# Kernel optimization log

Measured on AMD Instinct MI355X. Metric: run time of the kernel, lower is better.

## Reference

```python
import jax, jax.numpy as jnp
import numpy as np
import math

D_MODEL = 1024
HEADS = 16
D_K = D_MODEL // HEADS
D_FF = 2048
EPS = 1e-6


def layer_norm(x, alpha, bias):
    # torch.std uses unbiased estimator (ddof=1)
    m = x.mean(axis=-1, keepdims=True)
    var = ((x - m) ** 2).sum(axis=-1, keepdims=True) / (x.shape[-1] - 1)
    return alpha * (x - m) / (jnp.sqrt(var) + EPS) + bias


def setup_inputs() -> dict:
    key = jax.random.key(0)
    ks = jax.random.split(key, 12)
    s = 1.0 / math.sqrt(D_MODEL)
    return {
        "x": jax.random.normal(ks[0], (2, 2048, D_MODEL), dtype=jnp.float32),
        "mask": jnp.ones((2, 1, 1, 2048), dtype=jnp.float32),
        "Wq": jax.random.uniform(ks[1], (D_MODEL, D_MODEL), minval=-s, maxval=s),
        "Wk": jax.random.uniform(ks[2], (D_MODEL, D_MODEL), minval=-s, maxval=s),
        "Wv": jax.random.uniform(ks[3], (D_MODEL, D_MODEL), minval=-s, maxval=s),
        "Wo": jax.random.uniform(ks[4], (D_MODEL, D_MODEL), minval=-s, maxval=s),
        "bo": jnp.zeros((D_MODEL,), dtype=jnp.float32),
        "W1": jax.random.uniform(ks[5], (D_MODEL, D_FF), minval=-s, maxval=s),
        "b1": jnp.zeros((D_FF,), dtype=jnp.float32),
        "W2": jax.random.uniform(ks[6], (D_FF, D_MODEL), minval=-1.0 / math.sqrt(D_FF), maxval=1.0 / math.sqrt(D_FF)),
        "b2": jnp.zeros((D_MODEL,), dtype=jnp.float32),
        "ln1_a": jnp.ones((D_MODEL,), dtype=jnp.float32),
        "ln1_b": jnp.zeros((D_MODEL,), dtype=jnp.float32),
        "ln2_a": jnp.ones((D_MODEL,), dtype=jnp.float32),
        "ln2_b": jnp.zeros((D_MODEL,), dtype=jnp.float32),
    }


def reference(x, mask, Wq, Wk, Wv, Wo, bo, W1, b1, W2, b2, ln1_a, ln1_b, ln2_a, ln2_b):
    B, S, _ = x.shape
    # --- attention sublayer (pre-LN) ---
    x2 = layer_norm(x, ln1_a, ln1_b)
    q = (x2 @ Wq).reshape(B, S, HEADS, D_K).transpose(0, 2, 1, 3)  # [B,H,S,dk]
    k = (x2 @ Wk).reshape(B, S, HEADS, D_K).transpose(0, 2, 1, 3)
    v = (x2 @ Wv).reshape(B, S, HEADS, D_K).transpose(0, 2, 1, 3)
    attn = jnp.einsum("bhqd,bhkd->bhqk", q, k) / math.sqrt(D_K)
    attn = attn * mask                                  # multiplicative mask
    attn = jnp.where(attn == 0.0, -jnp.inf, attn)       # masked_fill(==0, -inf)
    scores = jax.nn.softmax(attn, axis=-1)
    av = jnp.einsum("bhqk,bhkd->bhqd", scores, v)
    concat = av.transpose(0, 2, 1, 3).reshape(B, S, D_MODEL)
    x = x + (concat @ Wo + bo)
    # --- FFN sublayer (pre-LN) ---
    x2 = layer_norm(x, ln2_a, ln2_b)
    h = jax.nn.relu(x2 @ W1 + b1)
    x = x + (h @ W2 + b2)
    return x
```

## Files before the change

kernel.cpp:

```cpp
#include <hip/hip_runtime.h>
#include <hip/hip_bf16.h>

typedef unsigned short u16;
typedef __attribute__((ext_vector_type(4))) float f32x4;
typedef __attribute__((ext_vector_type(8))) short bf16x8;

#define SEQ 2048
#define DM 1024
#define DKK 64
#define NH 16
#define DFF 2048
#define TOK 4096

#define AS1 __attribute__((address_space(1)))
#define AS3 __attribute__((address_space(3)))

#define MFMA16(a, b, c) __builtin_amdgcn_mfma_f32_16x16x32_bf16((a), (b), (c), 0, 0, 0)

__device__ __forceinline__ u16 f2b(float f) {
  unsigned u = __float_as_uint(f);
  u = u + 0x7fffu + ((u >> 16) & 1u);
  return (u16)(u >> 16);
}

__device__ __forceinline__ unsigned cvtpk(float lo, float hi) {
  unsigned r;
  asm("v_cvt_pk_bf16_f32 %0, %1, %2" : "=v"(r) : "v"(lo), "v"(hi));
  return r;
}

__device__ __forceinline__ void gload_lds16(const u16* g, u16* l) {
  __builtin_amdgcn_global_load_lds((AS1 unsigned*)(size_t)g, (AS3 unsigned*)l, 16, 0, 0);
}

__global__ __launch_bounds__(256)
void transpose_all(const float* __restrict__ Wq, const float* __restrict__ Wk,
                   const float* __restrict__ Wv, const float* __restrict__ Wo,
                   const float* __restrict__ W1, const float* __restrict__ W2,
                   u16* __restrict__ Wqkt, u16* __restrict__ Wvt, u16* __restrict__ Wot,
                   u16* __restrict__ W1t, u16* __restrict__ W2t) {
  const int bid = blockIdx.x;
  const float* src;
  u16* dst;
  int K, N, lb;
  if (bid < 1024)      { src = Wq; dst = Wqkt;                 K = 1024; N = 1024; lb = bid; }
  else if (bid < 2048) { src = Wk; dst = Wqkt + (1 << 20);     K = 1024; N = 1024; lb = bid - 1024; }
  else if (bid < 3072) { src = Wv; dst = Wvt;                  K = 1024; N = 1024; lb = bid - 2048; }
  else if (bid < 4096) { src = Wo; dst = Wot;                  K = 1024; N = 1024; lb = bid - 3072; }
  else if (bid < 6144) { src = W1; dst = W1t;                  K = 1024; N = 2048; lb = bid - 4096; }
  else                 { src = W2; dst = W2t;                  K = 2048; N = 1024; lb = bid - 6144; }
  const int nx = N / 32;
  const int n0 = (lb % nx) * 32, k0 = (lb / nx) * 32;
  __shared__ float t[32][33];
  const int tx = threadIdx.x, ty = threadIdx.y;
#pragma unroll
  for (int i = 0; i < 4; i++) {
    int k = ty + i * 8;
    t[k][tx] = src[(size_t)(k0 + k) * N + n0 + tx];
  }
  __syncthreads();
#pragma unroll
  for (int i = 0; i < 4; i++) {
    int n = ty + i * 8;
    dst[(size_t)(n0 + n) * K + k0 + tx] = f2b(t[tx][n]);
  }
}

__global__ __launch_bounds__(256)
void ln_kernel(const float* __restrict__ x, const float* __restrict__ alpha,
               const float* __restrict__ beta, u16* __restrict__ out) {
  const int row = blockIdx.x;
  const float4 v = ((const float4*)(x + (size_t)row * DM))[threadIdx.x];
  float s = v.x + v.y + v.z + v.w;
  float q = v.x * v.x + v.y * v.y + v.z * v.z + v.w * v.w;
#pragma unroll
  for (int off = 1; off < 64; off <<= 1) {
    s += __shfl_xor(s, off);
    q += __shfl_xor(q, off);
  }
  __shared__ float ss[4], qq[4];
  const int wid = threadIdx.x >> 6;
  if ((threadIdx.x & 63) == 0) { ss[wid] = s; qq[wid] = q; }
  __syncthreads();
  s = ss[0] + ss[1] + ss[2] + ss[3];
  q = qq[0] + qq[1] + qq[2] + qq[3];
  const float mean = s * (1.f / DM);
  float var = (q - (float)DM * mean * mean) * (1.f / (DM - 1));
  var = fmaxf(var, 0.f);
  const float inv = 1.f / (sqrtf(var) + 1e-6f);
  const float4 a4 = ((const float4*)alpha)[threadIdx.x];
  const float4 b4 = ((const float4*)beta)[threadIdx.x];
  ushort4 o;
  o.x = f2b((v.x - mean) * inv * a4.x + b4.x);
  o.y = f2b((v.y - mean) * inv * a4.y + b4.y);
  o.z = f2b((v.z - mean) * inv * a4.z + b4.z);
  o.w = f2b((v.w - mean) * inv * a4.w + b4.w);
  ((ushort4*)(out + (size_t)row * DM))[threadIdx.x] = o;
}

template <int MODE, int BM, int BN>
__global__ __launch_bounds__(256, 2)
void gemm_bt(const u16* __restrict__ A, const u16* __restrict__ Bt,
             int M, int N, int K,
             const float* __restrict__ bias, const float* __restrict__ res,
             void* __restrict__ outp, float oscale) {
  constexpr int AccM = BM / 32;
  constexpr int AccN = BN / 32;
  constexpr int L = (BM == 128 ? 2 : 1) + (BN == 128 ? 2 : 1);
  __shared__ alignas(16) u16 As[3][BM * 32];
  __shared__ alignas(16) u16 Bs[3][BN * 32];
  const int bm = blockIdx.x * BM, bn = blockIdx.y * BN;
  const int tid = threadIdx.x;
  const int lane = tid & 63, w = tid >> 6;
  const int wm = (w >> 1) * (BM / 2), wn = (w & 1) * (BN / 2);
  const int r = lane & 15, g = lane >> 4;
  const int srow = tid >> 2, skk = (tid & 3) * 8;

  f32x4 acc[AccM][AccN];
#pragma unroll
  for (int i = 0; i < AccM; i++)
#pragma unroll
    for (int j = 0; j < AccN; j++) acc[i][j] = (f32x4){0.f, 0.f, 0.f, 0.f};

  const u16* aP = A + (size_t)(bm + srow) * K + skk;
  const u16* bP = Bt + (size_t)(bn + srow) * K + skk;

  auto stage = [&](int kt, int buf) {
    gload_lds16(aP + kt, &As[buf][0] + w * 512);
    if (BM == 128) gload_lds16(aP + (size_t)64 * K + kt, &As[buf][0] + w * 512 + 2048);
    gload_lds16(bP + kt, &Bs[buf][0] + w * 512);
    if (BN == 128) gload_lds16(bP + (size_t)64 * K + kt, &Bs[buf][0] + w * 512 + 2048);
  };
  auto waitL = [&]() {
    if constexpr (L == 4) asm volatile("s_waitcnt vmcnt(4) lgkmcnt(0)" ::: "memory");
    else if constexpr (L == 3) asm volatile("s_waitcnt vmcnt(3) lgkmcnt(0)" ::: "memory");
    else asm volatile("s_waitcnt vmcnt(2) lgkmcnt(0)" ::: "memory");
  };
  auto compute = [&](int buf) {
    bf16x8 af[AccM], bfr[AccN];
#pragma unroll
    for (int i = 0; i < AccM; i++) af[i] = *(const bf16x8*)(&As[buf][(wm + i * 16 + r) * 32 + g * 8]);
#pragma unroll
    for (int j = 0; j < AccN; j++) bfr[j] = *(const bf16x8*)(&Bs[buf][(wn + j * 16 + r) * 32 + g * 8]);
#pragma unroll
    for (int i = 0; i < AccM; i++)
#pragma unroll
      for (int j = 0; j < AccN; j++) acc[i][j] = MFMA16(af[i], bfr[j], acc[i][j]);
  };

  const int NKT = K / 32;
  stage(0, 0);
  stage(32, 1);
  waitL();
  __builtin_amdgcn_s_barrier();
  __builtin_amdgcn_sched_barrier(0);
  for (int it = 0; it < NKT - 2; ++it) {
    stage((it + 2) * 32, (it + 2) % 3);
    compute(it % 3);
    waitL();
    __builtin_amdgcn_s_barrier();
    __builtin_amdgcn_sched_barrier(0);
  }
  compute((NKT - 2) % 3);
  asm volatile("s_waitcnt vmcnt(0) lgkmcnt(0)" ::: "memory");
  __builtin_amdgcn_s_barrier();
  __builtin_amdgcn_sched_barrier(0);
  compute((NKT - 1) % 3);

#pragma unroll
  for (int i = 0; i < AccM; i++)
#pragma unroll
    for (int j = 0; j < AccN; j++)
#pragma unroll
      for (int t = 0; t < 4; t++) {
        const int mg = bm + wm + i * 16 + g * 4 + t;
        const int ng = bn + wn + j * 16 + r;
        const float v = acc[i][j][t];
        if (MODE == 0) {
          const int which = ng >> 10, col = ng & 1023;
          const int bb = mg >> 11, ssx = mg & 2047, hh = col >> 6, dd = col & 63;
          const float sc = which ? 1.f : oscale;
          ((u16*)outp)[(size_t)which * (TOK * (size_t)DM) +
                       ((size_t)(bb * NH + hh) * SEQ + ssx) * DKK + dd] = f2b(v * sc);
        } else if (MODE == 1) {
          const int hh = mg >> 6, dd = mg & 63, bb = ng >> 11, ssx = ng & 2047;
          ((u16*)outp)[((size_t)(bb * NH + hh) * DKK + dd) * SEQ + ssx] = f2b(v);
        } else if (MODE == 2) {
          ((float*)outp)[(size_t)mg * N + ng] = res[(size_t)mg * N + ng] + v + bias[ng];
        } else {
          const float hv = v + bias[ng];
          ((u16*)outp)[(size_t)mg * N + ng] = f2b(hv > 0.f ? hv : 0.f);
        }
      }
}

__global__ __launch_bounds__(256, 4)
void attn_kernel(const u16* __restrict__ Q, const u16* __restrict__ Kb,
                 const u16* __restrict__ Vt, const float* __restrict__ mask,
                 u16* __restrict__ outc) {
  const int bid = blockIdx.x;
  const int bh = (bid & 7) * 4 + ((bid >> 3) & 3);
  const int qt = bid >> 5;
  const int b = bh >> 4, h = bh & 15;
  const int tid = threadIdx.x, lane = tid & 63, w = tid >> 6;
  const int r = lane & 15, g = lane >> 4;
  const int qbase = qt * 64 + w * 16;
  const u16* Qp = Q + ((size_t)bh * SEQ + qbase) * DKK;
  const u16* Kp = Kb + (size_t)bh * SEQ * DKK;
  const u16* Vp = Vt + (size_t)bh * DKK * SEQ;
  const float* mk = mask + b * SEQ;

  const bf16x8 bq0 = *(const bf16x8*)(Qp + r * DKK + g * 8);
  const bf16x8 bq1 = *(const bf16x8*)(Qp + r * DKK + 32 + g * 8);

  __shared__ __align__(16) u16 Ks[2][64 * 64];
  __shared__ __align__(16) u16 Vs[2][64 * 64];

  const int srow8 = lane >> 3;
  const int sgr = (lane & 7) ^ srow8;
  const u16* kSrc1 = Kp + (size_t)(w * 16 + srow8) * DKK + sgr * 8;
  const u16* kSrc2 = kSrc1 + 8 * DKK;
  const u16* vSrc1 = Vp + (size_t)(w * 16 + srow8) * SEQ + sgr * 8;
  const u16* vSrc2 = vSrc1 + 8 * SEQ;

  f32x4 o[4];
#pragma unroll
  for (int i = 0; i < 4; i++) o[i] = (f32x4){0.f, 0.f, 0.f, 0.f};
  float lr = 0.f;
  const int keyr = r & 7;

  gload_lds16(kSrc1, &Ks[0][0] + w * 1024);
  gload_lds16(kSrc2, &Ks[0][0] + w * 1024 + 512);
  gload_lds16(vSrc1, &Vs[0][0] + w * 1024);
  gload_lds16(vSrc2, &Vs[0][0] + w * 1024 + 512);
  asm volatile("s_waitcnt vmcnt(0)" ::: "memory");
  __builtin_amdgcn_s_barrier();
  __builtin_amdgcn_sched_barrier(0);

  const int NT = SEQ / 64;
  for (int it = 0; it < NT; ++it) {
    const int buf = it & 1;
    if (it + 1 < NT) {
      const int nsk = (it + 1) * 64;
      u16* kd = &Ks[buf ^ 1][0] + w * 1024;
      gload_lds16(kSrc1 + (size_t)nsk * DKK, kd);
      gload_lds16(kSrc2 + (size_t)nsk * DKK, kd + 512);
      u16* vd = &Vs[buf ^ 1][0] + w * 1024;
      gload_lds16(vSrc1 + nsk, vd);
      gload_lds16(vSrc2 + nsk, vd + 512);
    }

    f32x4 s[4];
    __builtin_amdgcn_s_setprio(1);
#pragma unroll
    for (int ks = 0; ks < 4; ks++) {
      const bf16x8 ka0 = *(const bf16x8*)&Ks[buf][(ks * 16 + r) * 64 + ((g ^ keyr) << 3)];
      const bf16x8 ka1 = *(const bf16x8*)&Ks[buf][(ks * 16 + r) * 64 + (((g + 4) ^ keyr) << 3)];
      f32x4 z = (f32x4){0.f, 0.f, 0.f, 0.f};
      z = MFMA16(ka0, bq0, z);
      z = MFMA16(ka1, bq1, z);
      s[ks] = z;
    }
    __builtin_amdgcn_s_setprio(0);

    const int sk = it * 64;
    float p[16];
    float rs = 0.f;
#pragma unroll
    for (int ks = 0; ks < 4; ks++) {
      const float4 mm = *(const float4*)(mk + sk + ks * 16 + 4 * g);
      float pr0 = s[ks][0] * mm.x, pr1 = s[ks][1] * mm.y;
      float pr2 = s[ks][2] * mm.z, pr3 = s[ks][3] * mm.w;
      float e0 = __builtin_amdgcn_exp2f(pr0), e1 = __builtin_amdgcn_exp2f(pr1);
      float e2 = __builtin_amdgcn_exp2f(pr2), e3 = __builtin_amdgcn_exp2f(pr3);
      e0 = (pr0 == 0.f) ? 0.f : e0;
      e1 = (pr1 == 0.f) ? 0.f : e1;
      e2 = (pr2 == 0.f) ? 0.f : e2;
      e3 = (pr3 == 0.f) ? 0.f : e3;
      p[ks * 4 + 0] = e0; p[ks * 4 + 1] = e1; p[ks * 4 + 2] = e2; p[ks * 4 + 3] = e3;
      rs += e0 + e1 + e2 + e3;
    }
    rs += __shfl_xor(rs, 16);
    rs += __shfl_xor(rs, 32);
    lr += rs;

    unsigned wk[4][2];
#pragma unroll
    for (int ks = 0; ks < 4; ks++) {
      wk[ks][0] = cvtpk(p[ks * 4 + 0], p[ks * 4 + 1]);
      wk[ks][1] = cvtpk(p[ks * 4 + 2], p[ks * 4 + 3]);
    }
    bf16x8 pa[2];
#pragma unroll
    for (int hh2 = 0; hh2 < 2; hh2++) {
      union { unsigned u[4]; bf16x8 v; } pu;
#pragma unroll
      for (int c = 0; c < 4; c++) {
        const int srcl = r + ((g & 1) * 2 + (c >> 1)) * 16;
        const unsigned lo = __shfl(wk[2 * hh2][c & 1], srcl);
        const unsigned hi = __shfl(wk[2 * hh2 + 1][c & 1], srcl);
        pu.u[c] = (g < 2) ? lo : hi;
      }
      pa[hh2] = pu.v;
    }

    __builtin_amdgcn_s_setprio(1);
#pragma unroll
    for (int dc = 0; dc < 4; dc++) {
      const int vr = dc * 16 + r;
      const bf16x8 bv0 = *(const bf16x8*)&Vs[buf][vr * 64 + ((g ^ keyr) << 3)];
      const bf16x8 bv1 = *(const bf16x8*)&Vs[buf][vr * 64 + (((g + 4) ^ keyr) << 3)];
      o[dc] = MFMA16(pa[0], bv0, o[dc]);
      o[dc] = MFMA16(pa[1], bv1, o[dc]);
    }
    __builtin_amdgcn_s_setprio(0);

    asm volatile("s_waitcnt vmcnt(0) lgkmcnt(0)" ::: "memory");
    __builtin_amdgcn_s_barrier();
    __builtin_amdgcn_sched_barrier(0);
  }

  float lq[4];
#pragma unroll
  for (int t = 0; t < 4; t++) lq[t] = __shfl(lr, 4 * g + t);
#pragma unroll
  for (int dc = 0; dc < 4; dc++)
#pragma unroll
    for (int t = 0; t < 4; t++) {
      const int srow_g = qbase + g * 4 + t;
      outc[((size_t)(b * SEQ + srow_g)) * DM + h * DKK + dc * 16 + r] = f2b(o[dc][t] / lq[t]);
    }
}

extern "C" void kernel_launch(void* const* d_in, const int* in_sizes, int n_in,
                              void* d_out, int out_size, void* d_ws, size_t ws_size,
                              hipStream_t stream) {
  const float* x    = (const float*)d_in[0];
  const float* mask = (const float*)d_in[1];
  const float* Wq   = (const float*)d_in[2];
  const float* Wk   = (const float*)d_in[3];
  const float* Wv   = (const float*)d_in[4];
  const float* Wo   = (const float*)d_in[5];
  const float* bo   = (const float*)d_in[6];
  const float* W1   = (const float*)d_in[7];
  const float* b1   = (const float*)d_in[8];
  const float* W2   = (const float*)d_in[9];
  const float* b2   = (const float*)d_in[10];
  const float* l1a  = (const float*)d_in[11];
  const float* l1b  = (const float*)d_in[12];
  const float* l2a  = (const float*)d_in[13];
  const float* l2b  = (const float*)d_in[14];

  char* wsb = (char*)d_ws;
  u16* Wqkt = (u16*)(wsb + (0ull << 20));
  u16* Wvt  = (u16*)(wsb + (4ull << 20));
  u16* Wot  = (u16*)(wsb + (6ull << 20));
  u16* W1t  = (u16*)(wsb + (8ull << 20));
  u16* W2t  = (u16*)(wsb + (12ull << 20));
  u16* x2   = (u16*)(wsb + (16ull << 20));
  u16* qkb  = (u16*)(wsb + (24ull << 20));
  u16* vtb  = (u16*)(wsb + (40ull << 20));
  float* x1 = (float*)(wsb + (48ull << 20));
  u16* concat = x2;
  u16* x2b = qkb;
  u16* hb  = (u16*)(wsb + (32ull << 20));

  const float qscale = 0.125f * 1.4426950408889634f;

  transpose_all<<<dim3(8192), dim3(32, 8), 0, stream>>>(Wq, Wk, Wv, Wo, W1, W2,
                                                        Wqkt, Wvt, Wot, W1t, W2t);

  ln_kernel<<<TOK, 256, 0, stream>>>(x, l1a, l1b, x2);

  gemm_bt<0, 128, 128><<<dim3(TOK / 128, 2048 / 128), 256, 0, stream>>>(
      x2, Wqkt, TOK, 2048, DM, nullptr, nullptr, qkb, qscale);
  gemm_bt<1, 64, 128><<<dim3(DM / 64, TOK / 128), 256, 0, stream>>>(
      Wvt, x2, DM, TOK, DM, nullptr, nullptr, vtb, 1.0f);

  attn_kernel<<<dim3(1024), 256, 0, stream>>>(qkb, qkb + (size_t)TOK * DM, vtb, mask, concat);

  gemm_bt<2, 128, 64><<<dim3(TOK / 128, DM / 64), 256, 0, stream>>>(
      concat, Wot, TOK, DM, DM, bo, x, x1, 1.0f);

  ln_kernel<<<TOK, 256, 0, stream>>>(x1, l2a, l2b, x2b);

  gemm_bt<3, 128, 128><<<dim3(TOK / 128, DFF / 128), 256, 0, stream>>>(
      x2b, W1t, TOK, DFF, DM, b1, nullptr, hb, 1.0f);
  gemm_bt<2, 128, 64><<<dim3(TOK / 128, DM / 64), 256, 0, stream>>>(
      hb, W2t, TOK, DM, DFF, b2, x1, (float*)d_out, 1.0f);
}
```

Baseline: 228.5 us.

## Restructure attention as split-K per wave and retile GEMMs with XCD-aware swizzle

```diff
diff --git a/kernel.cpp b/kernel.cpp
--- a/kernel.cpp
+++ b/kernel.cpp
@@ -99,17 +99,20 @@
 }
 
 template <int MODE, int BM, int BN>
-__global__ __launch_bounds__(256, 2)
+__global__ __launch_bounds__(256, 4)
 void gemm_bt(const u16* __restrict__ A, const u16* __restrict__ Bt,
              int M, int N, int K,
              const float* __restrict__ bias, const float* __restrict__ res,
-             void* __restrict__ outp, float oscale) {
+             void* __restrict__ outp, float oscale, int nm) {
   constexpr int AccM = BM / 32;
   constexpr int AccN = BN / 32;
   constexpr int L = (BM == 128 ? 2 : 1) + (BN == 128 ? 2 : 1);
   __shared__ alignas(16) u16 As[3][BM * 32];
   __shared__ alignas(16) u16 Bs[3][BN * 32];
-  const int bm = blockIdx.x * BM, bn = blockIdx.y * BN;
+  const int nwg = gridDim.x;
+  const int cpx = nwg >> 3;
+  const int wg = (blockIdx.x & 7) * cpx + (blockIdx.x >> 3);
+  const int bm = (wg % nm) * BM, bn = (wg / nm) * BN;
   const int tid = threadIdx.x;
   const int lane = tid & 63, w = tid >> 6;
   const int wm = (w >> 1) * (BM / 2), wn = (w & 1) * (BN / 2);
@@ -194,7 +197,7 @@
       }
 }
 
-__global__ __launch_bounds__(256, 4)
+__global__ __launch_bounds__(256, 2)
 void attn_kernel(const u16* __restrict__ Q, const u16* __restrict__ Kb,
                  const u16* __restrict__ Vt, const float* __restrict__ mask,
                  u16* __restrict__ outc) {
@@ -204,132 +207,177 @@
   const int b = bh >> 4, h = bh & 15;
   const int tid = threadIdx.x, lane = tid & 63, w = tid >> 6;
   const int r = lane & 15, g = lane >> 4;
-  const int qbase = qt * 64 + w * 16;
+  const int qbase = qt * 64;
   const u16* Qp = Q + ((size_t)bh * SEQ + qbase) * DKK;
   const u16* Kp = Kb + (size_t)bh * SEQ * DKK;
   const u16* Vp = Vt + (size_t)bh * DKK * SEQ;
-  const float* mk = mask + b * SEQ;
-
-  const bf16x8 bq0 = *(const bf16x8*)(Qp + r * DKK + g * 8);
-  const bf16x8 bq1 = *(const bf16x8*)(Qp + r * DKK + 32 + g * 8);
-
-  __shared__ __align__(16) u16 Ks[2][64 * 64];
-  __shared__ __align__(16) u16 Vs[2][64 * 64];
+  const int wk0 = w * 512;
+  const float* mk = mask + b * SEQ + wk0;
+
+  bf16x8 bq0[4], bq1[4];
+#pragma unroll
+  for (int qf = 0; qf < 4; qf++) {
+    bq0[qf] = *(const bf16x8*)(Qp + (size_t)(qf * 16 + r) * DKK + g * 8);
+    bq1[qf] = *(const bf16x8*)(Qp + (size_t)(qf * 16 + r) * DKK + 32 + g * 8);
+  }
+
+  __shared__ __align__(16) char KV[4][2][8192];
+  u16* const K0p = (u16*)&KV[w][0][0];
+  u16* const K1p = (u16*)&KV[w][1][0];
+  u16* const V0p = (u16*)&KV[w][0][4096];
+  u16* const V1p = (u16*)&KV[w][1][4096];
+  __shared__ float lrL[4][4][16];
 
   const int srow8 = lane >> 3;
   const int sgr = (lane & 7) ^ srow8;
-  const u16* kSrc1 = Kp + (size_t)(w * 16 + srow8) * DKK + sgr * 8;
-  const u16* kSrc2 = kSrc1 + 8 * DKK;
-  const u16* vSrc1 = Vp + (size_t)(w * 16 + srow8) * SEQ + sgr * 8;
-  const u16* vSrc2 = vSrc1 + 8 * SEQ;
-
-  f32x4 o[4];
-#pragma unroll
-  for (int i = 0; i < 4; i++) o[i] = (f32x4){0.f, 0.f, 0.f, 0.f};
-  float lr = 0.f;
+  const u16* kS = Kp + (size_t)(wk0 + srow8) * DKK + sgr * 8;
+  const u16* vS = Vp + (size_t)(lane >> 2) * SEQ + wk0 + (lane & 3) * 8;
+
+  f32x4 o[4][4];
+#pragma unroll
+  for (int i = 0; i < 4; i++)
+#pragma unroll
+    for (int j = 0; j < 4; j++) o[i][j] = (f32x4){0.f, 0.f, 0.f, 0.f};
+  float lr[4] = {0.f, 0.f, 0.f, 0.f};
   const int keyr = r & 7;
 
-  gload_lds16(kSrc1, &Ks[0][0] + w * 1024);
-  gload_lds16(kSrc2, &Ks[0][0] + w * 1024 + 512);
-  gload_lds16(vSrc1, &Vs[0][0] + w * 1024);
-  gload_lds16(vSrc2, &Vs[0][0] + w * 1024 + 512);
-  asm volatile("s_waitcnt vmcnt(0)" ::: "memory");
-  __builtin_amdgcn_s_barrier();
-  __builtin_amdgcn_sched_barrier(0);
-
-  const int NT = SEQ / 64;
-  for (int it = 0; it < NT; ++it) {
-    const int buf = it & 1;
-    if (it + 1 < NT) {
-      const int nsk = (it + 1) * 64;
-      u16* kd = &Ks[buf ^ 1][0] + w * 1024;
-      gload_lds16(kSrc1 + (size_t)nsk * DKK, kd);
-      gload_lds16(kSrc2 + (size_t)nsk * DKK, kd + 512);
-      u16* vd = &Vs[buf ^ 1][0] + w * 1024;
-      gload_lds16(vSrc1 + nsk, vd);
-      gload_lds16(vSrc2 + nsk, vd + 512);
+  gload_lds16(kS, K0p);
+  gload_lds16(kS + (size_t)8 * DKK, K0p + 512);
+  gload_lds16(kS + (size_t)16 * DKK, K0p + 1024);
+  gload_lds16(kS + (size_t)24 * DKK, K0p + 1536);
+  gload_lds16(vS, V0p);
+  gload_lds16(vS + (size_t)16 * SEQ, V0p + 512);
+  gload_lds16(vS + (size_t)32 * SEQ, V0p + 1024);
+  gload_lds16(vS + (size_t)48 * SEQ, V0p + 1536);
+
+#define ATILE(T, KP, VP, KPN, VPN, HASNEXT)                                           \
+  do {                                                                                \
+    const int kk = (T) * 32;                                                          \
+    if (HASNEXT) {                                                                    \
+      const int nk = kk + 32;                                                         \
+      gload_lds16(kS + (size_t)nk * DKK, KPN);                                        \
+      gload_lds16(kS + (size_t)(nk + 8) * DKK, KPN + 512);                            \
+      gload_lds16(kS + (size_t)(nk + 16) * DKK, KPN + 1024);                          \
+      gload_lds16(kS + (size_t)(nk + 24) * DKK, KPN + 1536);                          \
+      gload_lds16(vS + nk, VPN);                                                      \
+      gload_lds16(vS + (size_t)16 * SEQ + nk, VPN + 512);                             \
+      gload_lds16(vS + (size_t)32 * SEQ + nk, VPN + 1024);                            \
+      gload_lds16(vS + (size_t)48 * SEQ + nk, VPN + 1536);                            \
+      asm volatile("s_waitcnt vmcnt(8)" ::: "memory");                                \
+    } else {                                                                          \
+      asm volatile("s_waitcnt vmcnt(0)" ::: "memory");                                \
+    }                                                                                 \
+    const bf16x8 ka0 = *(const bf16x8*)(KP + (size_t)(r)*64 + ((g ^ keyr) << 3));     \
+    const bf16x8 ka1 = *(const bf16x8*)(KP + (size_t)(r)*64 + (((g + 4) ^ keyr) << 3));\
+    const bf16x8 kb0 = *(const bf16x8*)(KP + (size_t)(16 + r) * 64 + ((g ^ keyr) << 3));\
+    const bf16x8 kb1 = *(const bf16x8*)(KP + (size_t)(16 + r) * 64 + (((g + 4) ^ keyr) << 3));\
+    f32x4 s0[4], s1[4];                                                               \
+    __builtin_amdgcn_s_setprio(1);                                                    \
+    _Pragma("unroll")                                                                 \
+    for (int qf = 0; qf < 4; qf++) {                                                  \
+      f32x4 z = (f32x4){0.f, 0.f, 0.f, 0.f};                                          \
+      z = MFMA16(ka0, bq0[qf], z);                                                    \
+      z = MFMA16(ka1, bq1[qf], z);                                                    \
+      s0[qf] = z;                                                                     \
+      f32x4 y = (f32x4){0.f, 0.f, 0.f, 0.f};                                          \
+      y = MFMA16(kb0, bq0[qf], y);                                                    \
+      y = MFMA16(kb1, bq1[qf], y);                                                    \
+      s1[qf] = y;                                                                     \
+    }                                                                                 \
+    __builtin_amdgcn_s_setprio(0);                                                    \
+    const float4 m0 = *(const float4*)(mk + kk + 4 * g);                              \
+    const float4 m1 = *(const float4*)(mk + kk + 16 + 4 * g);                         \
+    const int ones = (m0.x == 1.f) & (m0.y == 1.f) & (m0.z == 1.f) & (m0.w == 1.f) &  \
+                     (m1.x == 1.f) & (m1.y == 1.f) & (m1.z == 1.f) & (m1.w == 1.f);   \
+    const bool fastm = __all(ones);                                                   \
+    bf16x8 pa[4];                                                                     \
+    _Pragma("unroll")                                                                 \
+    for (int qf = 0; qf < 4; qf++) {                                                  \
+      float p[8];                                                                     \
+      if (fastm) {                                                                    \
+        p[0] = __builtin_amdgcn_exp2f(s0[qf][0]);                                     \
+        p[1] = __builtin_amdgcn_exp2f(s0[qf][1]);                                     \
+        p[2] = __builtin_amdgcn_exp2f(s0[qf][2]);                                     \
+        p[3] = __builtin_amdgcn_exp2f(s0[qf][3]);                                     \
+        p[4] = __builtin_amdgcn_exp2f(s1[qf][0]);                                     \
+        p[5] = __builtin_amdgcn_exp2f(s1[qf][1]);                                     \
+        p[6] = __builtin_amdgcn_exp2f(s1[qf][2]);                                     \
+        p[7] = __builtin_amdgcn_exp2f(s1[qf][3]);                                     \
+      } else {                                                                        \
+        float pr;                                                                     \
+        pr = s0[qf][0] * m0.x; p[0] = (pr == 0.f) ? 0.f : __builtin_amdgcn_exp2f(pr); \
+        pr = s0[qf][1] * m0.y; p[1] = (pr == 0.f) ? 0.f : __builtin_amdgcn_exp2f(pr); \
+        pr = s0[qf][2] * m0.z; p[2] = (pr == 0.f) ? 0.f : __builtin_amdgcn_exp2f(pr); \
+        pr = s0[qf][3] * m0.w; p[3] = (pr == 0.f) ? 0.f : __builtin_amdgcn_exp2f(pr); \
+        pr = s1[qf][0] * m1.x; p[4] = (pr == 0.f) ? 0.f : __builtin_amdgcn_exp2f(pr); \
+        pr = s1[qf][1] * m1.y; p[5] = (pr == 0.f) ? 0.f : __builtin_amdgcn_exp2f(pr); \
+        pr = s1[qf][2] * m1.z; p[6] = (pr == 0.f) ? 0.f : __builtin_amdgcn_exp2f(pr); \
+        pr = s1[qf][3] * m1.w; p[7] = (pr == 0.f) ? 0.f : __builtin_amdgcn_exp2f(pr); \
+      }                                                                               \
+      float rs = ((p[0] + p[1]) + (p[2] + p[3])) + ((p[4] + p[5]) + (p[6] + p[7]));   \
+      rs += __shfl_xor(rs, 16);                                                       \
+      rs += __shfl_xor(rs, 32);                                                       \
+      lr[qf] += rs;                                                                   \
+      const unsigned w0 = cvtpk(p[0], p[1]), w1 = cvtpk(p[2], p[3]);                  \
+      const unsigned w2 = cvtpk(p[4], p[5]), w3 = cvtpk(p[6], p[7]);                  \
+      union { unsigned u[4]; bf16x8 v; } pu;                                          \
+      _Pragma("unroll")                                                               \
+      for (int c = 0; c < 4; c++) {                                                   \
+        const int srcl = r + ((g & 1) * 2 + (c >> 1)) * 16;                           \
+        const unsigned lo = __shfl((c & 1) ? w1 : w0, srcl);                          \
+        const unsigned hi = __shfl((c & 1) ? w3 : w2, srcl);                          \
+        pu.u[c] = (g < 2) ? lo : hi;                                                  \
+      }                                                                               \
+      pa[qf] = pu.v;                                                                  \
+    }                                                                                 \
+    __builtin_amdgcn_s_setprio(1);                                                    \
+    _Pragma("unroll")                                                                 \
+    for (int dc = 0; dc < 4; dc++) {                                                  \
+      const bf16x8 bv = *(const bf16x8*)(VP + (size_t)(dc * 16 + r) * 32 + g * 8);    \
+      _Pragma("unroll")                                                               \
+      for (int qf = 0; qf < 4; qf++) o[qf][dc] = MFMA16(pa[qf], bv, o[qf][dc]);       \
+    }                                                                                 \
+    __builtin_amdgcn_s_setprio(0);                                                    \
+  } while (0)
+
+  for (int tt = 0; tt < 16; tt += 2) {
+    ATILE(tt, K0p, V0p, K1p, V1p, true);
+    ATILE(tt + 1, K1p, V1p, K0p, V0p, (tt < 14));
+  }
+#undef ATILE
+
+  float* mo = (float*)&KV[0][0][0];
+  float* mw = mo + w * 4096;
+#pragma unroll
+  for (int qf = 0; qf < 4; qf++)
+#pragma unroll
+    for (int dc = 0; dc < 4; dc++)
+      *(f32x4*)(mw + (size_t)((qf * 4 + dc) * 64 + lane) * 4) = o[qf][dc];
+  if (lane < 16) {
+#pragma unroll
+    for (int qf = 0; qf < 4; qf++) lrL[w][qf][lane] = lr[qf];
+  }
+  __syncthreads();
+
+  const int qf = w;
+  float lq[4];
+#pragma unroll
+  for (int t = 0; t < 4; t++)
+    lq[t] = ((lrL[0][qf][4 * g + t] + lrL[1][qf][4 * g + t]) +
+             (lrL[2][qf][4 * g + t] + lrL[3][qf][4 * g + t]));
+#pragma unroll
+  for (int dc = 0; dc < 4; dc++) {
+    f32x4 a0 = *(const f32x4*)(mo + 0 * 4096 + (size_t)((qf * 4 + dc) * 64 + lane) * 4);
+    f32x4 a1 = *(const f32x4*)(mo + 1 * 4096 + (size_t)((qf * 4 + dc) * 64 + lane) * 4);
+    f32x4 a2 = *(const f32x4*)(mo + 2 * 4096 + (size_t)((qf * 4 + dc) * 64 + lane) * 4);
+    f32x4 a3 = *(const f32x4*)(mo + 3 * 4096 + (size_t)((qf * 4 + dc) * 64 + lane) * 4);
+#pragma unroll
+    for (int t = 0; t < 4; t++) {
+      const float val = ((a0[t] + a1[t]) + (a2[t] + a3[t])) / lq[t];
+      const int srow_g = qbase + qf * 16 + g * 4 + t;
+      outc[((size_t)(b * SEQ + srow_g)) * DM + h * DKK + dc * 16 + r] = f2b(val);
     }
-
-    f32x4 s[4];
-    __builtin_amdgcn_s_setprio(1);
-#pragma unroll
-    for (int ks = 0; ks < 4; ks++) {
-      const bf16x8 ka0 = *(const bf16x8*)&Ks[buf][(ks * 16 + r) * 64 + ((g ^ keyr) << 3)];
-      const bf16x8 ka1 = *(const bf16x8*)&Ks[buf][(ks * 16 + r) * 64 + (((g + 4) ^ keyr) << 3)];
-      f32x4 z = (f32x4){0.f, 0.f, 0.f, 0.f};
-      z = MFMA16(ka0, bq0, z);
-      z = MFMA16(ka1, bq1, z);
-      s[ks] = z;
-    }
-    __builtin_amdgcn_s_setprio(0);
-
-    const int sk = it * 64;
-    float p[16];
-    float rs = 0.f;
-#pragma unroll
-    for (int ks = 0; ks < 4; ks++) {
-      const float4 mm = *(const float4*)(mk + sk + ks * 16 + 4 * g);
-      float pr0 = s[ks][0] * mm.x, pr1 = s[ks][1] * mm.y;
-      float pr2 = s[ks][2] * mm.z, pr3 = s[ks][3] * mm.w;
-      float e0 = __builtin_amdgcn_exp2f(pr0), e1 = __builtin_amdgcn_exp2f(pr1);
-      float e2 = __builtin_amdgcn_exp2f(pr2), e3 = __builtin_amdgcn_exp2f(pr3);
-      e0 = (pr0 == 0.f) ? 0.f : e0;
-      e1 = (pr1 == 0.f) ? 0.f : e1;
-      e2 = (pr2 == 0.f) ? 0.f : e2;
-      e3 = (pr3 == 0.f) ? 0.f : e3;
-      p[ks * 4 + 0] = e0; p[ks * 4 + 1] = e1; p[ks * 4 + 2] = e2; p[ks * 4 + 3] = e3;
-      rs += e0 + e1 + e2 + e3;
-    }
-    rs += __shfl_xor(rs, 16);
-    rs += __shfl_xor(rs, 32);
-    lr += rs;
-
-    unsigned wk[4][2];
-#pragma unroll
-    for (int ks = 0; ks < 4; ks++) {
-      wk[ks][0] = cvtpk(p[ks * 4 + 0], p[ks * 4 + 1]);
-      wk[ks][1] = cvtpk(p[ks * 4 + 2], p[ks * 4 + 3]);
-    }
-    bf16x8 pa[2];
-#pragma unroll
-    for (int hh2 = 0; hh2 < 2; hh2++) {
-      union { unsigned u[4]; bf16x8 v; } pu;
-#pragma unroll
-      for (int c = 0; c < 4; c++) {
-        const int srcl = r + ((g & 1) * 2 + (c >> 1)) * 16;
-        const unsigned lo = __shfl(wk[2 * hh2][c & 1], srcl);
-        const unsigned hi = __shfl(wk[2 * hh2 + 1][c & 1], srcl);
-        pu.u[c] = (g < 2) ? lo : hi;
-      }
-      pa[hh2] = pu.v;
-    }
-
-    __builtin_amdgcn_s_setprio(1);
-#pragma unroll
-    for (int dc = 0; dc < 4; dc++) {
-      const int vr = dc * 16 + r;
-      const bf16x8 bv0 = *(const bf16x8*)&Vs[buf][vr * 64 + ((g ^ keyr) << 3)];
-      const bf16x8 bv1 = *(const bf16x8*)&Vs[buf][vr * 64 + (((g + 4) ^ keyr) << 3)];
-      o[dc] = MFMA16(pa[0], bv0, o[dc]);
-      o[dc] = MFMA16(pa[1], bv1, o[dc]);
-    }
-    __builtin_amdgcn_s_setprio(0);
-
-    asm volatile("s_waitcnt vmcnt(0) lgkmcnt(0)" ::: "memory");
-    __builtin_amdgcn_s_barrier();
-    __builtin_amdgcn_sched_barrier(0);
-  }
-
-  float lq[4];
-#pragma unroll
-  for (int t = 0; t < 4; t++) lq[t] = __shfl(lr, 4 * g + t);
-#pragma unroll
-  for (int dc = 0; dc < 4; dc++)
-#pragma unroll
-    for (int t = 0; t < 4; t++) {
-      const int srow_g = qbase + g * 4 + t;
-      outc[((size_t)(b * SEQ + srow_g)) * DM + h * DKK + dc * 16 + r] = f2b(o[dc][t] / lq[t]);
-    }
+  }
 }
 
 extern "C" void kernel_launch(void* const* d_in, const int* in_sizes, int n_in,
@@ -372,20 +420,20 @@
 
   ln_kernel<<<TOK, 256, 0, stream>>>(x, l1a, l1b, x2);
 
-  gemm_bt<0, 128, 128><<<dim3(TOK / 128, 2048 / 128), 256, 0, stream>>>(
-      x2, Wqkt, TOK, 2048, DM, nullptr, nullptr, qkb, qscale);
-  gemm_bt<1, 64, 128><<<dim3(DM / 64, TOK / 128), 256, 0, stream>>>(
-      Wvt, x2, DM, TOK, DM, nullptr, nullptr, vtb, 1.0f);
+  gemm_bt<0, 64, 128><<<dim3(1024), 256, 0, stream>>>(
+      x2, Wqkt, TOK, 2048, DM, nullptr, nullptr, qkb, qscale, 64);
+  gemm_bt<1, 64, 64><<<dim3(1024), 256, 0, stream>>>(
+      Wvt, x2, DM, TOK, DM, nullptr, nullptr, vtb, 1.0f, 16);
 
   attn_kernel<<<dim3(1024), 256, 0, stream>>>(qkb, qkb + (size_t)TOK * DM, vtb, mask, concat);
 
-  gemm_bt<2, 128, 64><<<dim3(TOK / 128, DM / 64), 256, 0, stream>>>(
-      concat, Wot, TOK, DM, DM, bo, x, x1, 1.0f);
+  gemm_bt<2, 64, 64><<<dim3(1024), 256, 0, stream>>>(
+      concat, Wot, TOK, DM, DM, bo, x, x1, 1.0f, 64);
 
   ln_kernel<<<TOK, 256, 0, stream>>>(x1, l2a, l2b, x2b);
 
-  gemm_bt<3, 128, 128><<<dim3(TOK / 128, DFF / 128), 256, 0, stream>>>(
-      x2b, W1t, TOK, DFF, DM, b1, nullptr, hb, 1.0f);
-  gemm_bt<2, 128, 64><<<dim3(TOK / 128, DM / 64), 256, 0, stream>>>(
-      hb, W2t, TOK, DM, DFF, b2, x1, (float*)d_out, 1.0f);
-}
+  gemm_bt<3, 64, 128><<<dim3(1024), 256, 0, stream>>>(
+      x2b, W1t, TOK, DFF, DM, b1, nullptr, hb, 1.0f, 64);
+  gemm_bt<2, 64, 64><<<dim3(1024), 256, 0, stream>>>(
+      hb, W2t, TOK, DM, DFF, b2, x1, (float*)d_out, 1.0f, 64);
+}
```

New measurement: 227.7 us. About the same (-0.4%).
